# Kernel tuning notes

Measured on AMD Instinct MI355X. Metric: run time of the kernel, lower is better.

## Reference

```python
import jax, jax.numpy as jnp
import numpy as np

B, S, E, H = 2, 2048, 1024, 16
DH = E // H            # 64 head dim
ROT = DH // 2          # 32: RotaryEmbedding(head_dim//2) rotates first 32 dims only
CTX = 2048             # sliding KV window
THETA = 10000.0


def setup_inputs() -> dict:
    key = jax.random.key(0)
    ks = jax.random.split(key, 7)
    sc = 1.0 / np.sqrt(E)
    mk = lambda k, sh, s=1.0: (jax.random.normal(k, sh, jnp.float32) * s)
    return {
        "query": mk(ks[0], (B, S, E)),
        "key":   mk(ks[1], (B, S, E)),
        "value": mk(ks[2], (B, S, E)),
        "Wq": mk(ks[3], (E, E), sc), "bq": jnp.zeros((E,), jnp.float32),
        "Wk": mk(ks[4], (E, E), sc), "bk": jnp.zeros((E,), jnp.float32),
        "Wv": mk(ks[5], (E, E), sc), "bv": jnp.zeros((E,), jnp.float32),
        "Wo": mk(ks[6], (E, E), sc), "bo": jnp.zeros((E,), jnp.float32),
    }


def _rope(t):
    # t: [B, H, S, DH]; rotate first ROT dims, pass the rest through (offset=0).
    seq = t.shape[2]
    inv_freq = 1.0 / (THETA ** (jnp.arange(0, ROT, 2, dtype=jnp.float32) / ROT))  # [ROT//2]
    ang = jnp.arange(seq, dtype=jnp.float32)[:, None] * inv_freq[None, :]          # [S, ROT//2]
    cos = jnp.repeat(jnp.cos(ang), 2, axis=-1)  # [S, ROT] (pairwise-interleaved freqs)
    sin = jnp.repeat(jnp.sin(ang), 2, axis=-1)
    rot, rest = t[..., :ROT], t[..., ROT:]
    x1, x2 = rot[..., 0::2], rot[..., 1::2]
    rot_half = jnp.stack([-x2, x1], axis=-1).reshape(rot.shape)  # rotate_half on pairs
    return jnp.concatenate([rot * cos + rot_half * sin, rest], axis=-1)


def reference(query, key, value, Wq, bq, Wk, bk, Wv, bv, Wo, bo):
    def heads(x, W, b):
        return (x @ W.T + b).reshape(B, -1, H, DH).transpose(0, 2, 1, 3)  # [B,H,S,DH]

    q = _rope(heads(query, Wq, bq))
    k = _rope(heads(key, Wk, bk))
    v = heads(value, Wv, bv)
    k, v = k[:, :, -CTX:], v[:, :, -CTX:]  # sliding window (no-op when S == CTX)

    scale = jnp.float32(1.0 / np.sqrt(DH))
    scores = jnp.einsum('bhqd,bhkd->bhqk', q, k) * scale  # [B,H,Sq,Sk]
    sq, sk = q.shape[2], k.shape[2]
    causal = jnp.tril(jnp.ones((sk, sk), dtype=bool))[-sq:]  # [Sq,Sk]
    scores = jnp.where(causal[None, None], scores, jnp.float32(-jnp.inf))
    probs = jax.nn.softmax(scores, axis=-1)  # dropout=0 (eval)
    out = jnp.einsum('bhqk,bhkd->bhqd', probs, v)
    out = out.transpose(0, 2, 1, 3).reshape(B, -1, E)
    return out @ Wo.T + bo
```

## Files before the change

kernel.cpp:

```cpp
#include <hip/hip_runtime.h>
#include <stdint.h>
#include <math.h>

typedef __bf16 bf16x8 __attribute__((ext_vector_type(8)));
typedef float f32x4 __attribute__((ext_vector_type(4)));

__device__ __forceinline__ float bf2f(uint16_t x) {
  unsigned u = ((unsigned)x) << 16;
  float f;
  __builtin_memcpy(&f, &u, 4);
  return f;
}
__device__ __forceinline__ uint16_t f2bf(float f) {
  __bf16 h = (__bf16)f;
  uint16_t u;
  __builtin_memcpy(&u, &h, 2);
  return u;
}
__device__ __forceinline__ bf16x8 pack8(float4 lo, float4 hi) {
  bf16x8 v;
  v[0] = (__bf16)lo.x; v[1] = (__bf16)lo.y; v[2] = (__bf16)lo.z; v[3] = (__bf16)lo.w;
  v[4] = (__bf16)hi.x; v[5] = (__bf16)hi.y; v[6] = (__bf16)hi.z; v[7] = (__bf16)hi.w;
  return v;
}
__device__ __forceinline__ bf16x8 cvt8(const float* p) {
  return pack8(*(const float4*)p, *(const float4*)(p + 4));
}

typedef __attribute__((address_space(1))) const unsigned int gu32;
typedef __attribute__((address_space(3))) unsigned int lu32;
__device__ __forceinline__ void async_copy16(const void* gp, void* lp) {
  __builtin_amdgcn_global_load_lds((gu32*)gp, (lu32*)lp, 16, 0, 0);
}

__global__ __launch_bounds__(256) void cvt_kernel(
    const float* __restrict__ s0, uint16_t* __restrict__ d0,
    const float* __restrict__ s1, uint16_t* __restrict__ d1,
    const float* __restrict__ s2, uint16_t* __restrict__ d2,
    const float* __restrict__ s3, uint16_t* __restrict__ d3) {
  const int z = blockIdx.z;
  const float* s = z == 0 ? s0 : z == 1 ? s1 : z == 2 ? s2 : s3;
  uint16_t* d = z == 0 ? d0 : z == 1 ? d1 : z == 2 ? d2 : d3;
  const size_t idx = ((size_t)blockIdx.x * 256 + threadIdx.x) * 8;
  *(bf16x8*)(d + idx) = cvt8(s + idx);
}

template <bool A_F32, bool W_F32, bool C_F32, bool VT, bool ROPE, int BM, int NF>
__global__ __launch_bounds__(256) void gemm3_kernel(
    const void* __restrict__ A0, const void* __restrict__ W0,
    const float* __restrict__ b0, void* __restrict__ C0,
    const void* __restrict__ A1, const void* __restrict__ W1,
    const float* __restrict__ b1, void* __restrict__ C1,
    const void* __restrict__ A2, const void* __restrict__ W2,
    const float* __restrict__ b2, void* __restrict__ C2,
    int M, int N, int K) {
  constexpr int BN = NF * 32;
  constexpr int AF = BM / 32;
  const int z = blockIdx.z;
  const void* Av = z == 0 ? A0 : z == 1 ? A1 : A2;
  const void* Wp = z == 0 ? W0 : z == 1 ? W1 : W2;
  const float* bias = z == 0 ? b0 : z == 1 ? b1 : b2;
  void* Cv = z == 0 ? C0 : z == 1 ? C1 : C2;

  __shared__ __align__(16) uint16_t As[BM * 64];
  __shared__ __align__(16) uint16_t Bs[BN * 64];
  const int tid = threadIdx.x;
  const int wave = tid >> 6, lane = tid & 63;
  const int quad = lane >> 4, l16 = lane & 15;
  const int l = blockIdx.y * gridDim.x + blockIdx.x;
  const int nmt = M / BM;
  const int bm = (l % nmt) * BM;
  const int bn = (l / nmt) * BN;
  const int wm = (wave >> 1) * (BM / 2);
  const int wn = (wave & 1) * (BN / 2);

  f32x4 acc[AF][NF] = {};

  for (int k0 = 0; k0 < K; k0 += 64) {
    bf16x8 ar[AF], wr[NF];
    if (A_F32) {
#pragma unroll
      for (int i = 0; i < AF; i++) {
        const int c = i * 256 + tid;
        const int r = c >> 3, pc = ((c & 7) ^ (r & 7)) << 3;
        ar[i] = cvt8((const float*)Av + (size_t)(bm + r) * K + k0 + pc);
      }
    }
    if (W_F32) {
#pragma unroll
      for (int i = 0; i < NF; i++) {
        const int c = i * 256 + tid;
        const int r = c >> 3, pc = ((c & 7) ^ (r & 7)) << 3;
        wr[i] = cvt8((const float*)Wp + (size_t)(bn + r) * K + k0 + pc);
      }
    }
    if (k0) __syncthreads();
#pragma unroll
    for (int i = 0; i < AF; i++) {
      const int c = i * 256 + tid;
      const int r = c >> 3, pc = ((c & 7) ^ (r & 7)) << 3;
      if (A_F32) *(bf16x8*)(As + c * 8) = ar[i];
      else async_copy16((const uint16_t*)Av + (size_t)(bm + r) * K + k0 + pc,
                        As + (i * 256 + (tid & 192)) * 8);
    }
#pragma unroll
    for (int i = 0; i < NF; i++) {
      const int c = i * 256 + tid;
      const int r = c >> 3, pc = ((c & 7) ^ (r & 7)) << 3;
      if (W_F32) *(bf16x8*)(Bs + c * 8) = wr[i];
      else async_copy16((const uint16_t*)Wp + (size_t)(bn + r) * K + k0 + pc,
                        Bs + (i * 256 + (tid & 192)) * 8);
    }
    __syncthreads();
#pragma unroll
    for (int s = 0; s < 2; s++) {
      bf16x8 af[AF], bfr[NF];
#pragma unroll
      for (int i = 0; i < AF; i++) {
        const int Ra = wm + i * 16 + l16;
        af[i] = *(const bf16x8*)(As + Ra * 64 + (((s * 4 + quad) ^ (Ra & 7)) << 3));
      }
#pragma unroll
      for (int j = 0; j < NF; j++) {
        const int Rb = wn + j * 16 + l16;
        bfr[j] = *(const bf16x8*)(Bs + Rb * 64 + (((s * 4 + quad) ^ (Rb & 7)) << 3));
      }
#pragma unroll
      for (int i = 0; i < AF; i++)
#pragma unroll
        for (int j = 0; j < NF; j++)
          acc[i][j] = __builtin_amdgcn_mfma_f32_16x16x32_bf16(af[i], bfr[j], acc[i][j], 0, 0, 0);
    }
  }
  if (VT && z == 2) {
#pragma unroll
    for (int j = 0; j < NF; j++) {
      const int n = bn + wn + j * 16 + l16;
      const float bj = bias[n];
      const int h = n >> 6, dh = n & 63;
#pragma unroll
      for (int i = 0; i < AF; i++) {
        const int m0 = bm + wm + i * 16 + quad * 4;
        const int b = m0 >> 11, s0 = m0 & 2047;
        uint2 pk;
        pk.x = (unsigned)f2bf(acc[i][j][0] + bj) |
               ((unsigned)f2bf(acc[i][j][1] + bj) << 16);
        pk.y = (unsigned)f2bf(acc[i][j][2] + bj) |
               ((unsigned)f2bf(acc[i][j][3] + bj) << 16);
        *(uint2*)((uint16_t*)Cv + ((size_t)((b * 16 + h) * 64 + dh)) * 2048 + s0) = pk;
      }
    }
  } else {
#pragma unroll
    for (int j = 0; j < NF; j++) {
      const int n = bn + wn + j * 16 + l16;
      const float bj = bias[n];
      const int dh = (wn + j * 16 + l16) & 63;
      const bool rot = ROPE && (((wn + j * 16) & 63) < 32);
      float invrev = 0.f;
      if (rot)
        invrev = __expf(-0.5756462732485115f * (float)(dh >> 1)) *
                 0.15915494309189535f;
#pragma unroll
      for (int i = 0; i < AF; i++) {
        const int m0 = bm + wm + i * 16 + quad * 4;
#pragma unroll
        for (int r = 0; r < 4; r++) {
          float v = acc[i][j][r] + bj;
          if (rot) {
            const int s_pos = (m0 + r) & 2047;
            float rev = (float)s_pos * invrev;
            rev -= floorf(rev);
            const float sn = __builtin_amdgcn_sinf(rev);
            const float cs = __builtin_amdgcn_cosf(rev);
            const float partner = __shfl_xor(v, 1);
            v = (dh & 1) ? (v * cs + partner * sn) : (v * cs - partner * sn);
          }
          if (C_F32) ((float*)Cv)[(size_t)(m0 + r) * N + n] = v;
          else       ((uint16_t*)Cv)[(size_t)(m0 + r) * N + n] = f2bf(v);
        }
      }
    }
  }
}

__global__ __launch_bounds__(256) void flash_kernel(const uint16_t* __restrict__ Q,
                                                    const uint16_t* __restrict__ K,
                                                    const uint16_t* __restrict__ VT,
                                                    uint16_t* __restrict__ AO) {
  const int bx = blockIdx.x;
  const int xcd = bx & 7;
  const int slot = bx >> 3;
  const int bh = (slot >> 5) * 8 + xcd;
  const int qt = 31 - (slot & 31);
  const int h = bh & 15;
  const int b = bh >> 4;
  const int tid = threadIdx.x;
  const int wave = tid >> 6, lane = tid & 63;
  const int quad = lane >> 4, l16 = lane & 15;

  __shared__ __align__(16) uint16_t Ks[64 * 64];
  __shared__ __align__(16) uint16_t Vt[64 * 64];
  __shared__ __align__(16) uint16_t Ps[4][16 * 72];

  const int qrow = qt * 64 + wave * 16 + l16;
  bf16x8 qf[2];
#pragma unroll
  for (int s = 0; s < 2; s++) {
    union { bf16x8 v; uint16_t u[8]; } t0;
    t0.v = *(const bf16x8*)(Q + ((size_t)(b * 2048 + qrow) * 1024) + h * 64 + s * 32 + quad * 8);
#pragma unroll
    for (int j = 0; j < 8; j++) t0.u[j] = f2bf(bf2f(t0.u[j]) * 0.125f);
    qf[s] = t0.v;
  }

  const size_t vbase = ((size_t)((b * 16 + h) * 64)) * 2048;

  float lsum = 0.f;
  f32x4 o[4] = {};

  const int nkt = qt + 1;
  for (int kt = 0; kt < nkt; kt++) {
    if (kt) __syncthreads();
#pragma unroll
    for (int i = 0; i < 2; i++) {
      const int c = i * 256 + tid;
      const int r = c >> 3, pc = ((c & 7) ^ (r & 7)) << 3;
      async_copy16(K + ((size_t)(b * 2048 + kt * 64 + r) * 1024) + h * 64 + pc,
                   Ks + (i * 256 + (tid & 192)) * 8);
      async_copy16(VT + vbase + (size_t)r * 2048 + kt * 64 + pc,
                   Vt + (i * 256 + (tid & 192)) * 8);
    }
    __syncthreads();

    f32x4 sacc[4] = {};
#pragma unroll
    for (int s = 0; s < 2; s++)
#pragma unroll
      for (int t = 0; t < 4; t++) {
        const int R = t * 16 + l16;
        bf16x8 kf = *(const bf16x8*)(Ks + R * 64 + (((s * 4 + quad) ^ (R & 7)) << 3));
        sacc[t] = __builtin_amdgcn_mfma_f32_16x16x32_bf16(kf, qf[s], sacc[t], 0, 0, 0);
      }
    if (kt == qt) {
#pragma unroll
      for (int t = 0; t < 4; t++)
#pragma unroll
        for (int r = 0; r < 4; r++)
          if (kt * 64 + t * 16 + quad * 4 + r > qrow) sacc[t][r] = -1e30f;
    }
#pragma unroll
    for (int t = 0; t < 4; t++) {
      float p0 = __expf(sacc[t][0]), p1 = __expf(sacc[t][1]);
      float p2 = __expf(sacc[t][2]), p3 = __expf(sacc[t][3]);
      lsum += (p0 + p1) + (p2 + p3);
      uint2 pk;
      pk.x = (unsigned)f2bf(p0) | ((unsigned)f2bf(p1) << 16);
      pk.y = (unsigned)f2bf(p2) | ((unsigned)f2bf(p3) << 16);
      *(uint2*)(&Ps[wave][l16 * 72 + t * 16 + quad * 4]) = pk;
    }
#pragma unroll
    for (int s = 0; s < 2; s++) {
      const bf16x8 pa = *(const bf16x8*)(&Ps[wave][l16 * 72 + s * 32 + quad * 8]);
#pragma unroll
      for (int t = 0; t < 4; t++) {
        const int R = t * 16 + l16;
        const bf16x8 vb = *(const bf16x8*)(Vt + R * 64 + (((s * 4 + quad) ^ (R & 7)) << 3));
        o[t] = __builtin_amdgcn_mfma_f32_16x16x32_bf16(pa, vb, o[t], 0, 0, 0);
      }
    }
  }
  lsum += __shfl_xor(lsum, 16);
  lsum += __shfl_xor(lsum, 32);
  const float inv = 1.f / lsum;
  float invr[4];
#pragma unroll
  for (int r = 0; r < 4; r++) invr[r] = __shfl(inv, quad * 4 + r);
#pragma unroll
  for (int t = 0; t < 4; t++)
#pragma unroll
    for (int r = 0; r < 4; r++) {
      const int qg = qt * 64 + wave * 16 + quad * 4 + r;
      AO[((size_t)(b * 2048 + qg) * 1024) + h * 64 + t * 16 + l16] =
          f2bf(o[t][r] * invr[r]);
    }
}

extern "C" void kernel_launch(void* const* d_in, const int* in_sizes, int n_in,
                              void* d_out, int out_size, void* d_ws, size_t ws_size,
                              hipStream_t stream) {
  const float* query = (const float*)d_in[0];
  const float* key   = (const float*)d_in[1];
  const float* value = (const float*)d_in[2];
  const float* Wq = (const float*)d_in[3];
  const float* bq = (const float*)d_in[4];
  const float* Wk = (const float*)d_in[5];
  const float* bk = (const float*)d_in[6];
  const float* Wv = (const float*)d_in[7];
  const float* bv = (const float*)d_in[8];
  const float* Wo = (const float*)d_in[9];
  const float* bo = (const float*)d_in[10];
  float* out = (float*)d_out;

  uint16_t* ws = (uint16_t*)d_ws;
  uint16_t* Qb  = ws;
  uint16_t* Kb  = ws + (size_t)4194304;
  uint16_t* VTb = ws + (size_t)8388608;
  uint16_t* AOb = ws + (size_t)12582912;

  dim3 blk(256);

  if (ws_size >= (size_t)64 * 1024 * 1024) {
    uint16_t* Qc  = ws + (size_t)16777216;
    uint16_t* Kc  = ws + (size_t)20971520;
    uint16_t* Vc  = ws + (size_t)25165824;
    uint16_t* Wqc = ws + (size_t)29360128;
    uint16_t* Wkc = ws + (size_t)30408704;
    uint16_t* Wvc = ws + (size_t)31457280;
    uint16_t* Woc = ws + (size_t)32505856;

    cvt_kernel<<<dim3(512, 1, 4), blk, 0, stream>>>(
        Wq, Wqc, Wk, Wkc, Wv, Wvc, Wo, Woc);
    cvt_kernel<<<dim3(2048, 1, 3), blk, 0, stream>>>(
        query, Qc, key, Kc, value, Vc, nullptr, nullptr);
    gemm3_kernel<false, false, false, true, true, 128, 4><<<dim3(8, 32, 3), blk, 0, stream>>>(
        Qc, Wqc, bq, Qb,
        Kc, Wkc, bk, Kb,
        Vc, Wvc, bv, VTb,
        4096, 1024, 1024);
    flash_kernel<<<dim3(1024), blk, 0, stream>>>(Qb, Kb, VTb, AOb);
    gemm3_kernel<false, false, true, false, false, 128, 2><<<dim3(16, 32, 1), blk, 0, stream>>>(
        AOb, Woc, bo, out,
        AOb, Woc, bo, out,
        AOb, Woc, bo, out,
        4096, 1024, 1024);
  } else {
    uint16_t* Wqc = AOb;
    uint16_t* Wkc = AOb + (size_t)1048576;
    uint16_t* Wvc = AOb + (size_t)2097152;
    cvt_kernel<<<dim3(512, 1, 3), blk, 0, stream>>>(
        Wq, Wqc, Wk, Wkc, Wv, Wvc, nullptr, nullptr);
    gemm3_kernel<true, false, false, true, true, 128, 2><<<dim3(16, 32, 3), blk, 0, stream>>>(
        query, Wqc, bq, Qb,
        key,   Wkc, bk, Kb,
        value, Wvc, bv, VTb,
        4096, 1024, 1024);
    flash_kernel<<<dim3(1024), blk, 0, stream>>>(Qb, Kb, VTb, AOb);
    gemm3_kernel<false, true, true, false, false, 128, 2><<<dim3(16, 32, 1), blk, 0, stream>>>(
        AOb, Wo, bo, out,
        AOb, Wo, bo, out,
        AOb, Wo, bo, out,
        4096, 1024, 1024);
  }
}
```

Measured before the change: 229.8 us.

## Use 128-row query tiles with 512-thread flash blocks and merge conversion launches

The flash attention kernel now runs 512-thread blocks covering 128 query rows, loading two 64-key tiles per sync so each K/V tile in LDS serves eight waves instead of four. The per-block sync count drops, and a per-wave skip avoids computing fully masked tiles. The softmax switches to exp2 with log2(e) folded into the Q scale. The separate weight and activation fp32->bf16 conversion launches are merged into one kernel. The risks are lower occupancy from larger blocks and fewer blocks (512), plus idle waves on the diagonal tiles.

```diff
diff --git a/kernel.cpp b/kernel.cpp
--- a/kernel.cpp
+++ b/kernel.cpp
@@ -42,6 +42,31 @@
   const float* s = z == 0 ? s0 : z == 1 ? s1 : z == 2 ? s2 : s3;
   uint16_t* d = z == 0 ? d0 : z == 1 ? d1 : z == 2 ? d2 : d3;
   const size_t idx = ((size_t)blockIdx.x * 256 + threadIdx.x) * 8;
+  *(bf16x8*)(d + idx) = cvt8(s + idx);
+}
+
+__global__ __launch_bounds__(256) void cvt_all_kernel(
+    const float* __restrict__ q, uint16_t* __restrict__ qo,
+    const float* __restrict__ k, uint16_t* __restrict__ ko,
+    const float* __restrict__ v, uint16_t* __restrict__ vo,
+    const float* __restrict__ w0, uint16_t* __restrict__ w0o,
+    const float* __restrict__ w1, uint16_t* __restrict__ w1o,
+    const float* __restrict__ w2, uint16_t* __restrict__ w2o,
+    const float* __restrict__ w3, uint16_t* __restrict__ w3o) {
+  const int z = blockIdx.z;
+  const float* s;
+  uint16_t* d;
+  size_t idx;
+  if (z < 3) {
+    s = z == 0 ? q : z == 1 ? k : v;
+    d = z == 0 ? qo : z == 1 ? ko : vo;
+    idx = ((size_t)blockIdx.x * 256 + threadIdx.x) * 8;
+  } else {
+    const int w = blockIdx.x >> 9;
+    s = w == 0 ? w0 : w == 1 ? w1 : w == 2 ? w2 : w3;
+    d = w == 0 ? w0o : w == 1 ? w1o : w == 2 ? w2o : w3o;
+    idx = ((size_t)(blockIdx.x & 511) * 256 + threadIdx.x) * 8;
+  }
   *(bf16x8*)(d + idx) = cvt8(s + idx);
 }
 
@@ -184,89 +209,105 @@
   }
 }
 
-__global__ __launch_bounds__(256) void flash_kernel(const uint16_t* __restrict__ Q,
+__global__ __launch_bounds__(512) void flash_kernel(const uint16_t* __restrict__ Q,
                                                     const uint16_t* __restrict__ K,
                                                     const uint16_t* __restrict__ VT,
                                                     uint16_t* __restrict__ AO) {
   const int bx = blockIdx.x;
   const int xcd = bx & 7;
   const int slot = bx >> 3;
-  const int bh = (slot >> 5) * 8 + xcd;
-  const int qt = 31 - (slot & 31);
+  const int bh = (slot >> 4) * 8 + xcd;
+  const int qt2 = (slot < 32) ? (15 - (slot & 15)) : (slot & 15);
   const int h = bh & 15;
   const int b = bh >> 4;
   const int tid = threadIdx.x;
   const int wave = tid >> 6, lane = tid & 63;
   const int quad = lane >> 4, l16 = lane & 15;
 
-  __shared__ __align__(16) uint16_t Ks[64 * 64];
-  __shared__ __align__(16) uint16_t Vt[64 * 64];
-  __shared__ __align__(16) uint16_t Ps[4][16 * 72];
-
-  const int qrow = qt * 64 + wave * 16 + l16;
+  __shared__ __align__(16) uint16_t Ks[2][64 * 64];
+  __shared__ __align__(16) uint16_t Vt[2][64 * 64];
+  __shared__ __align__(16) uint16_t Ps[8][16 * 72];
+
+  const float QS = 0.18033688011112042f;
+  const int qrowMin = qt2 * 128 + wave * 16;
+  const int qrowMax = qrowMin + 15;
+  const int qrow = qrowMin + l16;
   bf16x8 qf[2];
 #pragma unroll
   for (int s = 0; s < 2; s++) {
     union { bf16x8 v; uint16_t u[8]; } t0;
     t0.v = *(const bf16x8*)(Q + ((size_t)(b * 2048 + qrow) * 1024) + h * 64 + s * 32 + quad * 8);
 #pragma unroll
-    for (int j = 0; j < 8; j++) t0.u[j] = f2bf(bf2f(t0.u[j]) * 0.125f);
+    for (int j = 0; j < 8; j++) t0.u[j] = f2bf(bf2f(t0.u[j]) * QS);
     qf[s] = t0.v;
   }
 
   const size_t vbase = ((size_t)((b * 16 + h) * 64)) * 2048;
+
+  const int sr = tid >> 3;
+  const int spc = ((tid & 7) ^ (sr & 7)) << 3;
+  const int sld = (tid & 448) * 8;
 
   float lsum = 0.f;
   f32x4 o[4] = {};
 
-  const int nkt = qt + 1;
-  for (int kt = 0; kt < nkt; kt++) {
-    if (kt) __syncthreads();
-#pragma unroll
-    for (int i = 0; i < 2; i++) {
-      const int c = i * 256 + tid;
-      const int r = c >> 3, pc = ((c & 7) ^ (r & 7)) << 3;
-      async_copy16(K + ((size_t)(b * 2048 + kt * 64 + r) * 1024) + h * 64 + pc,
-                   Ks + (i * 256 + (tid & 192)) * 8);
-      async_copy16(VT + vbase + (size_t)r * 2048 + kt * 64 + pc,
-                   Vt + (i * 256 + (tid & 192)) * 8);
+  const int nkt = 2 * qt2 + 2;
+  for (int outer = 0; outer < nkt; outer += 2) {
+    if (outer) __syncthreads();
+#pragma unroll
+    for (int sub = 0; sub < 2; sub++) {
+      const int kt = outer + sub;
+      async_copy16(K + ((size_t)(b * 2048 + kt * 64 + sr) * 1024) + h * 64 + spc,
+                   Ks[sub] + sld);
+      async_copy16(VT + vbase + (size_t)sr * 2048 + kt * 64 + spc,
+                   Vt[sub] + sld);
     }
     __syncthreads();
 
-    f32x4 sacc[4] = {};
-#pragma unroll
-    for (int s = 0; s < 2; s++)
+#pragma unroll
+    for (int sub = 0; sub < 2; sub++) {
+      const int kt = outer + sub;
+      if (kt * 64 > qrowMax) continue;
+      const uint16_t* ksp = Ks[sub];
+      const uint16_t* vtp = Vt[sub];
+
+      f32x4 sacc[4] = {};
+#pragma unroll
+      for (int s = 0; s < 2; s++)
+#pragma unroll
+        for (int t = 0; t < 4; t++) {
+          const int R = t * 16 + l16;
+          bf16x8 kf = *(const bf16x8*)(ksp + R * 64 + (((s * 4 + quad) ^ (R & 7)) << 3));
+          sacc[t] = __builtin_amdgcn_mfma_f32_16x16x32_bf16(kf, qf[s], sacc[t], 0, 0, 0);
+        }
+      if (kt * 64 + 63 > qrowMin) {
+#pragma unroll
+        for (int t = 0; t < 4; t++)
+#pragma unroll
+          for (int r = 0; r < 4; r++)
+            if (kt * 64 + t * 16 + quad * 4 + r > qrow) sacc[t][r] = -1e30f;
+      }
 #pragma unroll
       for (int t = 0; t < 4; t++) {
-        const int R = t * 16 + l16;
-        bf16x8 kf = *(const bf16x8*)(Ks + R * 64 + (((s * 4 + quad) ^ (R & 7)) << 3));
-        sacc[t] = __builtin_amdgcn_mfma_f32_16x16x32_bf16(kf, qf[s], sacc[t], 0, 0, 0);
-      }
-    if (kt == qt) {
-#pragma unroll
-      for (int t = 0; t < 4; t++)
-#pragma unroll
-        for (int r = 0; r < 4; r++)
-          if (kt * 64 + t * 16 + quad * 4 + r > qrow) sacc[t][r] = -1e30f;
-    }
-#pragma unroll
-    for (int t = 0; t < 4; t++) {
-      float p0 = __expf(sacc[t][0]), p1 = __expf(sacc[t][1]);
-      float p2 = __expf(sacc[t][2]), p3 = __expf(sacc[t][3]);
-      lsum += (p0 + p1) + (p2 + p3);
-      uint2 pk;
-      pk.x = (unsigned)f2bf(p0) | ((unsigned)f2bf(p1) << 16);
-      pk.y = (unsigned)f2bf(p2) | ((unsigned)f2bf(p3) << 16);
-      *(uint2*)(&Ps[wave][l16 * 72 + t * 16 + quad * 4]) = pk;
-    }
-#pragma unroll
-    for (int s = 0; s < 2; s++) {
-      const bf16x8 pa = *(const bf16x8*)(&Ps[wave][l16 * 72 + s * 32 + quad * 8]);
-#pragma unroll
-      for (int t = 0; t < 4; t++) {
-        const int R = t * 16 + l16;
-        const bf16x8 vb = *(const bf16x8*)(Vt + R * 64 + (((s * 4 + quad) ^ (R & 7)) << 3));
-        o[t] = __builtin_amdgcn_mfma_f32_16x16x32_bf16(pa, vb, o[t], 0, 0, 0);
+        float p0 = __builtin_amdgcn_exp2f(sacc[t][0]);
+        float p1 = __builtin_amdgcn_exp2f(sacc[t][1]);
+        float p2 = __builtin_amdgcn_exp2f(sacc[t][2]);
+        float p3 = __builtin_amdgcn_exp2f(sacc[t][3]);
+        lsum += (p0 + p1) + (p2 + p3);
+        uint2 pk;
+        pk.x = (unsigned)f2bf(p0) | ((unsigned)f2bf(p1) << 16);
+        pk.y = (unsigned)f2bf(p2) | ((unsigned)f2bf(p3) << 16);
+        *(uint2*)(&Ps[wave][l16 * 72 + t * 16 + quad * 4]) = pk;
+      }
+#pragma unroll
+      for (int s = 0; s < 2; s++) {
+        const bf16x8 pa = *(const bf16x8*)(&Ps[wave][l16 * 72 + s * 32 + quad * 8]);
+#pragma unroll
+        for (int t = 0; t < 4; t++) {
+          const int R = t * 16 + l16;
+          const bf16x8 vb = *(const bf16x8*)(vtp + R * 64 + (((s * 4 + quad) ^ (R & 7)) << 3));
+          o[t] = __builtin_amdgcn_mfma_f32_16x16x32_bf16(pa, vb, o[t], 0, 0, 0);
+        }
       }
     }
   }
@@ -280,7 +321,7 @@
   for (int t = 0; t < 4; t++)
 #pragma unroll
     for (int r = 0; r < 4; r++) {
-      const int qg = qt * 64 + wave * 16 + quad * 4 + r;
+      const int qg = qrowMin + quad * 4 + r;
       AO[((size_t)(b * 2048 + qg) * 1024) + h * 64 + t * 16 + l16] =
           f2bf(o[t][r] * invr[r]);
     }
@@ -309,6 +350,7 @@
   uint16_t* AOb = ws + (size_t)12582912;
 
   dim3 blk(256);
+  dim3 fblk(512);
 
   if (ws_size >= (size_t)64 * 1024 * 1024) {
     uint16_t* Qc  = ws + (size_t)16777216;
@@ -319,16 +361,15 @@
     uint16_t* Wvc = ws + (size_t)31457280;
     uint16_t* Woc = ws + (size_t)32505856;
 
-    cvt_kernel<<<dim3(512, 1, 4), blk, 0, stream>>>(
+    cvt_all_kernel<<<dim3(2048, 1, 4), blk, 0, stream>>>(
+        query, Qc, key, Kc, value, Vc,
         Wq, Wqc, Wk, Wkc, Wv, Wvc, Wo, Woc);
-    cvt_kernel<<<dim3(2048, 1, 3), blk, 0, stream>>>(
-        query, Qc, key, Kc, value, Vc, nullptr, nullptr);
     gemm3_kernel<false, false, false, true, true, 128, 4><<<dim3(8, 32, 3), blk, 0, stream>>>(
         Qc, Wqc, bq, Qb,
         Kc, Wkc, bk, Kb,
         Vc, Wvc, bv, VTb,
         4096, 1024, 1024);
-    flash_kernel<<<dim3(1024), blk, 0, stream>>>(Qb, Kb, VTb, AOb);
+    flash_kernel<<<dim3(512), fblk, 0, stream>>>(Qb, Kb, VTb, AOb);
     gemm3_kernel<false, false, true, false, false, 128, 2><<<dim3(16, 32, 1), blk, 0, stream>>>(
         AOb, Woc, bo, out,
         AOb, Woc, bo, out,
@@ -345,7 +386,7 @@
         key,   Wkc, bk, Kb,
         value, Wvc, bv, VTb,
         4096, 1024, 1024);
-    flash_kernel<<<dim3(1024), blk, 0, stream>>>(Qb, Kb, VTb, AOb);
+    flash_kernel<<<dim3(512), fblk, 0, stream>>>(Qb, Kb, VTb, AOb);
     gemm3_kernel<false, true, true, false, false, 128, 2><<<dim3(16, 32, 1), blk, 0, stream>>>(
         AOb, Wo, bo, out,
         AOb, Wo, bo, out,
```

After: 207.4 us. 1.11x faster.
